# Kernel optimization log

Measured on AMD Instinct MI355X. Metric: run time of the kernel, lower is better.

Reference implementation:

```python
import math
import jax, jax.numpy as jnp
import numpy as np

H = 8
C_HIDDEN = 32
C_Q = 256


def setup_inputs() -> dict:
    key = jax.random.key(0)
    ks = jax.random.split(key, 9)
    B, S, Q, K = 1, 128, 256, 256
    q_x = jax.random.normal(ks[0], (B, S, Q, C_Q), dtype=jnp.float32)
    kv_x = jax.random.normal(ks[1], (B, S, K, C_Q), dtype=jnp.float32)
    bias1 = jax.random.normal(ks[2], (B, S, 1, 1, K), dtype=jnp.float32)
    bias2 = jax.random.normal(ks[3], (B, 1, H, Q, K), dtype=jnp.float32)
    scale = 1.0 / math.sqrt(C_Q)
    wq = jax.random.normal(ks[4], (H * C_HIDDEN, C_Q), dtype=jnp.float32) * scale
    wk = jax.random.normal(ks[5], (H * C_HIDDEN, C_Q), dtype=jnp.float32) * scale
    wv = jax.random.normal(ks[6], (H * C_HIDDEN, C_Q), dtype=jnp.float32) * scale
    wg = jax.random.normal(ks[7], (H * C_HIDDEN, C_Q), dtype=jnp.float32) * scale
    wo = jax.random.normal(ks[8], (C_Q, H * C_HIDDEN), dtype=jnp.float32) * scale
    return {"q_x": q_x, "kv_x": kv_x, "bias1": bias1, "bias2": bias2,
            "wq": wq, "wk": wk, "wv": wv, "wg": wg, "wo": wo}


def _split_heads(x):
    # [..., L, H*c] -> [..., H, L, c]
    y = x.reshape(x.shape[:-1] + (H, C_HIDDEN))
    return jnp.moveaxis(y, -2, -3)


def reference(q_x, kv_x, bias1, bias2, wq, wk, wv, wg, wo):
    # QKV projections (no bias), per-head split, scale q by 1/sqrt(c_hidden)
    q = _split_heads(q_x @ wq.T) / math.sqrt(C_HIDDEN)   # [B,S,H,Q,c]
    k = _split_heads(kv_x @ wk.T)                         # [B,S,H,K,c]
    v = _split_heads(kv_x @ wv.T)                         # [B,S,H,K,c]
    # attention logits with additive biases folded in
    a = jnp.einsum('...hqc,...hkc->...hqk', q, k) + bias1 + bias2
    a = jax.nn.softmax(a, axis=-1)
    o = jnp.einsum('...hqk,...hkc->...hqc', a, v)         # [B,S,H,Q,c]
    o = jnp.moveaxis(o, -3, -2)                           # [B,S,Q,H,c]
    # sigmoid gating from query data
    g = jax.nn.sigmoid(q_x @ wg.T)                        # [B,S,Q,H*c]
    g = g.reshape(g.shape[:-1] + (H, C_HIDDEN))
    o = o * g
    o = o.reshape(o.shape[:-2] + (H * C_HIDDEN,))         # flatten heads
    return o @ wo.T                                       # [B,S,Q,C_Q]
```

## Files before the change

### kernel.cpp

```cpp
#include <hip/hip_runtime.h>
#include <math.h>

#define S_DIM 128
#define H_DIM 8
#define M_TOT (S_DIM * 256)

typedef unsigned short ushort_t;
typedef unsigned int   uint32;
typedef __bf16  v8bf  __attribute__((ext_vector_type(8)));
typedef float   v4f   __attribute__((ext_vector_type(4)));

__device__ inline ushort_t f2b(float x) {
    unsigned int u = __float_as_uint(x);
    u += 0x7fffu + ((u >> 16) & 1u);
    return (ushort_t)(u >> 16);
}
__device__ inline float b2f(ushort_t h) {
    return __uint_as_float(((unsigned int)h) << 16);
}

#define GLDS16(gp, lp) __builtin_amdgcn_global_load_lds( \
    (const __attribute__((address_space(1))) void*)(gp), \
    (__attribute__((address_space(3))) void*)(lp), 16, 0, 0)

__global__ __launch_bounds__(256) void split_x(
    const float* __restrict__ xq, const float* __restrict__ xkv,
    ushort_t* __restrict__ hi, ushort_t* __restrict__ lo)
{
    const size_t BUF4 = (size_t)M_TOT * 64;
    const float* src = blockIdx.y ? xkv : xq;
    size_t base = (size_t)blockIdx.y * BUF4;
    int i = blockIdx.x * 256 + threadIdx.x;
    float4 v = ((const float4*)src)[i];
    ushort4 h, l;
    h.x = f2b(v.x); l.x = f2b(v.x - b2f(h.x));
    h.y = f2b(v.y); l.y = f2b(v.y - b2f(h.y));
    h.z = f2b(v.z); l.z = f2b(v.z - b2f(h.z));
    h.w = f2b(v.w); l.w = f2b(v.w - b2f(h.w));
    ((ushort4*)hi)[base + i] = h;
    ((ushort4*)lo)[base + i] = l;
}

__global__ __launch_bounds__(256) void split_w(
    const float* __restrict__ w0, const float* __restrict__ w1,
    const float* __restrict__ w2, const float* __restrict__ w3,
    const float* __restrict__ w4,
    ushort_t* __restrict__ hi, ushort_t* __restrict__ lo)
{
    const float* src;
    switch (blockIdx.y) {
        case 0: src = w0; break; case 1: src = w1; break;
        case 2: src = w2; break; case 3: src = w3; break;
        default: src = w4; break;
    }
    int i = blockIdx.x * 256 + threadIdx.x;
    float4 v = ((const float4*)src)[i];
    ushort4 h, l;
    h.x = f2b(v.x); l.x = f2b(v.x - b2f(h.x));
    h.y = f2b(v.y); l.y = f2b(v.y - b2f(h.y));
    h.z = f2b(v.z); l.z = f2b(v.z - b2f(h.z));
    h.w = f2b(v.w); l.w = f2b(v.w - b2f(h.w));
    size_t base = (size_t)blockIdx.y * 16384;
    ((ushort4*)hi)[base + i] = h;
    ((ushort4*)lo)[base + i] = l;
}


__global__ __launch_bounds__(256) void gemm_proj(
    const ushort_t* __restrict__ Xhi, const ushort_t* __restrict__ Xlo,
    const ushort_t* __restrict__ Whi4, const ushort_t* __restrict__ Wlo4,
    ushort_t* __restrict__ qh, ushort_t* __restrict__ ql,
    ushort_t* __restrict__ kh, ushort_t* __restrict__ kl,
    float* __restrict__ g_out,
    ushort_t* __restrict__ vh,
    float qscale)
{
    __shared__ ushort_t lds[4][128 * 32];

    const int z    = blockIdx.z;
    const int L    = blockIdx.x + 4 * blockIdx.y;
    const int mti  = ((L >> 5) << 3) + (L & 7);
    const int nti  = (L >> 3) & 3;
    const int t    = threadIdx.x;
    const int l    = t & 63;
    const int wv   = t >> 6;
    const int wm   = wv & 1;
    const int wn   = wv >> 1;
    const int idx  = l & 15;
    const int quad = l >> 4;
    const int m0   = mti * 128;
    const int n0   = nti * 128;

    const size_t BUF = (size_t)M_TOT * 256;
    const ushort_t* Ahi = Xhi + (size_t)z * BUF;
    const ushort_t* Alo = Xlo + (size_t)z * BUF;
    const ushort_t* Whi = Whi4 + (size_t)z * 131072;
    const ushort_t* Wlo = Wlo4 + (size_t)z * 131072;
    const float scale = z ? 1.f : qscale;

    const ushort_t* srcs[4] = { Ahi + (size_t)m0 * 256, Alo + (size_t)m0 * 256,
                                Whi + (size_t)n0 * 256, Wlo + (size_t)n0 * 256 };

    v4f acc[4][4];
    #pragma unroll
    for (int i = 0; i < 4; ++i)
        #pragma unroll
        for (int j = 0; j < 4; ++j) acc[i][j] = (v4f){0.f, 0.f, 0.f, 0.f};

    for (int k0 = 0; k0 < 256; k0 += 32) {
        #pragma unroll
        for (int b = 0; b < 4; ++b) {
            #pragma unroll
            for (int i = 0; i < 2; ++i) {
                const int sb   = wv * 128 + i * 64;
                const int slot = sb + l;
                const int row  = slot >> 2;
                const int gseg = ((slot & 3) - (row >> 1)) & 3;
                const ushort_t* g = srcs[b] + (size_t)row * 256 + k0 + gseg * 8;
                GLDS16(g, &lds[b][sb * 8]);
            }
        }
        __builtin_amdgcn_s_waitcnt(0);
        __syncthreads();

        v8bf ah[4], al[4], bh[4], bl[4];
        #pragma unroll
        for (int mt = 0; mt < 4; ++mt) {
            const int r   = wm * 64 + mt * 16 + idx;
            const int off = r * 32 + (((quad + (r >> 1)) & 3) << 3);
            ah[mt] = *(const v8bf*)&lds[0][off];
            al[mt] = *(const v8bf*)&lds[1][off];
        }
        #pragma unroll
        for (int nt = 0; nt < 4; ++nt) {
            const int r   = wn * 64 + nt * 16 + idx;
            const int off = r * 32 + (((quad + (r >> 1)) & 3) << 3);
            bh[nt] = *(const v8bf*)&lds[2][off];
            bl[nt] = *(const v8bf*)&lds[3][off];
        }

        #pragma unroll
        for (int mt = 0; mt < 4; ++mt)
            #pragma unroll
            for (int nt = 0; nt < 4; ++nt) {
                acc[mt][nt] = __builtin_amdgcn_mfma_f32_16x16x32_bf16(ah[mt], bh[nt], acc[mt][nt], 0, 0, 0);
                acc[mt][nt] = __builtin_amdgcn_mfma_f32_16x16x32_bf16(al[mt], bh[nt], acc[mt][nt], 0, 0, 0);
                acc[mt][nt] = __builtin_amdgcn_mfma_f32_16x16x32_bf16(ah[mt], bl[nt], acc[mt][nt], 0, 0, 0);
            }
        __syncthreads();
    }

    ushort_t* dsth = z ? kh : qh;
    ushort_t* dstl = z ? kl : ql;

    #pragma unroll
    for (int mt = 0; mt < 4; ++mt) {
        const int mbase = m0 + wm * 64 + mt * 16 + quad * 4;
        const int s = mbase >> 8, r8 = mbase & 255;
        #pragma unroll
        for (int nt = 0; nt < 4; ++nt) {
            const int gcol = n0 + wn * 64 + nt * 16 + idx;
            if (gcol < 256) {
                const int hh = gcol >> 5, c = gcol & 31;
                const size_t di = (((size_t)(s * 8 + hh) * 256) + r8) * 32 + c;
                #pragma unroll
                for (int r = 0; r < 4; ++r) {
                    const float val = acc[mt][nt][r] * scale;
                    const ushort_t hv = f2b(val);
                    dsth[di + (size_t)r * 32] = hv;
                    dstl[di + (size_t)r * 32] = f2b(val - b2f(hv));
                }
            } else if (z == 0) {
                const int gc = gcol - 256;
                #pragma unroll
                for (int r = 0; r < 4; ++r)
                    g_out[(size_t)(mbase + r) * 256 + gc] = acc[mt][nt][r];
            } else {
                const int gc = gcol - 256, hh = gc >> 5, c = gc & 31;
                ushort4 hv4;
                #pragma unroll
                for (int r = 0; r < 4; ++r)
                    ((ushort_t*)&hv4)[r] = f2b(acc[mt][nt][r]);
                const size_t di = (((size_t)(s * 8 + hh) * 32) + c) * 256 + r8;
                *(ushort4*)&vh[di] = hv4;
            }
        }
    }
}

__global__ __launch_bounds__(256) void gemm_out(
    const ushort_t* __restrict__ Ah, const ushort_t* __restrict__ Whi,
    const ushort_t* __restrict__ Wlo, float* __restrict__ Cf)
{
    __shared__ ushort_t lds[3][128 * 32];

    const int L    = blockIdx.x + 2 * blockIdx.y;
    const int mti  = ((L >> 4) << 3) + (L & 7);
    const int nti  = (L >> 3) & 1;
    const int t    = threadIdx.x;
    const int l    = t & 63;
    const int wv   = t >> 6;
    const int wm   = wv & 1;
    const int wn   = wv >> 1;
    const int idx  = l & 15;
    const int quad = l >> 4;
    const int m0   = mti * 128;
    const int n0   = nti * 128;

    const ushort_t* srcs[3] = { Ah + (size_t)m0 * 256,
                                Whi + (size_t)n0 * 256, Wlo + (size_t)n0 * 256 };

    v4f acc[4][4];
    #pragma unroll
    for (int i = 0; i < 4; ++i)
        #pragma unroll
        for (int j = 0; j < 4; ++j) acc[i][j] = (v4f){0.f, 0.f, 0.f, 0.f};

    for (int k0 = 0; k0 < 256; k0 += 32) {
        #pragma unroll
        for (int b = 0; b < 3; ++b) {
            #pragma unroll
            for (int i = 0; i < 2; ++i) {
                const int sb   = wv * 128 + i * 64;
                const int slot = sb + l;
                const int row  = slot >> 2;
                const int gseg = ((slot & 3) - (row >> 1)) & 3;
                const ushort_t* g = srcs[b] + (size_t)row * 256 + k0 + gseg * 8;
                GLDS16(g, &lds[b][sb * 8]);
            }
        }
        __builtin_amdgcn_s_waitcnt(0);
        __syncthreads();

        v8bf ah[4], bh[4], bl[4];
        #pragma unroll
        for (int mt = 0; mt < 4; ++mt) {
            const int r   = wm * 64 + mt * 16 + idx;
            const int off = r * 32 + (((quad + (r >> 1)) & 3) << 3);
            ah[mt] = *(const v8bf*)&lds[0][off];
        }
        #pragma unroll
        for (int nt = 0; nt < 4; ++nt) {
            const int r   = wn * 64 + nt * 16 + idx;
            const int off = r * 32 + (((quad + (r >> 1)) & 3) << 3);
            bh[nt] = *(const v8bf*)&lds[1][off];
            bl[nt] = *(const v8bf*)&lds[2][off];
        }

        #pragma unroll
        for (int mt = 0; mt < 4; ++mt)
            #pragma unroll
            for (int nt = 0; nt < 4; ++nt) {
                acc[mt][nt] = __builtin_amdgcn_mfma_f32_16x16x32_bf16(ah[mt], bh[nt], acc[mt][nt], 0, 0, 0);
                acc[mt][nt] = __builtin_amdgcn_mfma_f32_16x16x32_bf16(ah[mt], bl[nt], acc[mt][nt], 0, 0, 0);
            }
        __syncthreads();
    }

    #pragma unroll
    for (int mt = 0; mt < 4; ++mt) {
        #pragma unroll
        for (int nt = 0; nt < 4; ++nt) {
            const int gcol = n0 + wn * 64 + nt * 16 + idx;
            #pragma unroll
            for (int r = 0; r < 4; ++r) {
                const int grow = m0 + wm * 64 + mt * 16 + quad * 4 + r;
                Cf[(size_t)grow * 256 + gcol] = acc[mt][nt][r];
            }
        }
    }
}

__global__ __launch_bounds__(256, 2) void attn_mfma(
    const ushort_t* __restrict__ qh, const ushort_t* __restrict__ ql,
    const ushort_t* __restrict__ kh, const ushort_t* __restrict__ kl,
    const ushort_t* __restrict__ vth,
    const float* __restrict__ b1, const float* __restrict__ b2,
    const float* __restrict__ gbuf,
    ushort_t* __restrict__ oh)
{
    __shared__ __align__(16) uint32   pbuf[4][64 * 36];
    __shared__ __align__(16) ushort_t kst[2][3][2048];
    __shared__ __align__(16) float    invl[4][64];

    const int sh = blockIdx.x, s = sh >> 3, h = sh & 7;
    const int t = threadIdx.x, l = t & 63, w = t >> 6;
    const int idx = l & 15, quad = l >> 4;

    const size_t shb = (size_t)sh * 8192;
    const ushort_t* qhp = qh + shb;
    const ushort_t* qlp = ql + shb;
    const ushort_t* khp = kh + shb;
    const ushort_t* klp = kl + shb;
    const ushort_t* vhp = vth + shb;
    const float* b1p = b1 + (size_t)s * 256;
    const float* b2p = b2 + (size_t)h * 65536;

    const int ksrow = t >> 2;
    const int ksseg = (( (t & 3) - (ksrow >> 1)) & 3);
    const int vsrow = t >> 3;
    const int vsseg = (( (t & 7) - (vsrow >> 1)) & 7);
    const size_t koff = (size_t)ksrow * 32 + ksseg * 8;
    const size_t voff = (size_t)vsrow * 256 + vsseg * 8;
    const int wbase = w * 512;

    v8bf qfh[4], qfl[4];
    #pragma unroll
    for (int nt = 0; nt < 4; ++nt) {
        const int off = (w * 64 + nt * 16 + idx) * 32 + quad * 8;
        qfh[nt] = *(const v8bf*)(qhp + off);
        qfl[nt] = *(const v8bf*)(qlp + off);
    }

    v4f oacc[4][2];
    #pragma unroll
    for (int mt = 0; mt < 4; ++mt) {
        oacc[mt][0] = (v4f){0.f, 0.f, 0.f, 0.f};
        oacc[mt][1] = (v4f){0.f, 0.f, 0.f, 0.f};
    }
    float lrun[4] = {0.f, 0.f, 0.f, 0.f};

    GLDS16(khp + koff, &kst[0][0][wbase]);
    GLDS16(klp + koff, &kst[0][1][wbase]);
    GLDS16(vhp + voff, &kst[0][2][wbase]);
    __builtin_amdgcn_s_waitcnt(0);
    __syncthreads();

    for (int c4 = 0; c4 < 4; ++c4) {
        const int ak0 = c4 * 64;
        const int cur = c4 & 1;

        if (c4 < 3) {
            const size_t nb = (size_t)(ak0 + 64) * 32;
            GLDS16(khp + nb + koff, &kst[cur ^ 1][0][wbase]);
            GLDS16(klp + nb + koff, &kst[cur ^ 1][1][wbase]);
            GLDS16(vhp + (ak0 + 64) + voff, &kst[cur ^ 1][2][wbase]);
        }

        v8bf kfh[4], kfl[4];
        #pragma unroll
        for (int at = 0; at < 4; ++at) {
            const int row = at * 16 + idx;
            const int off = row * 32 + (((quad + (row >> 1)) & 3) << 3);
            kfh[at] = *(const v8bf*)&kst[cur][0][off];
            kfl[at] = *(const v8bf*)&kst[cur][1][off];
        }

        v4f sacc[4][4];
        #pragma unroll
        for (int at = 0; at < 4; ++at)
            #pragma unroll
            for (int nt = 0; nt < 4; ++nt)
                sacc[at][nt] = (v4f){0.f, 0.f, 0.f, 0.f};
        __builtin_amdgcn_s_setprio(1);
        #pragma unroll
        for (int at = 0; at < 4; ++at)
            #pragma unroll
            for (int nt = 0; nt < 4; ++nt) {
                sacc[at][nt] = __builtin_amdgcn_mfma_f32_16x16x32_bf16(kfh[at], qfh[nt], sacc[at][nt], 0, 0, 0);
                sacc[at][nt] = __builtin_amdgcn_mfma_f32_16x16x32_bf16(kfl[at], qfh[nt], sacc[at][nt], 0, 0, 0);
                sacc[at][nt] = __builtin_amdgcn_mfma_f32_16x16x32_bf16(kfh[at], qfl[nt], sacc[at][nt], 0, 0, 0);
            }
        __builtin_amdgcn_s_setprio(0);

        v8bf vfh[2][2];
        #pragma unroll
        for (int n2 = 0; n2 < 2; ++n2)
            #pragma unroll
            for (int kt = 0; kt < 2; ++kt) {
                const int c  = n2 * 16 + idx;
                const int sp = ((kt * 4 + quad) + (c >> 1)) & 7;
                vfh[n2][kt] = *(const v8bf*)&kst[cur][2][c * 64 + sp * 8];
            }

        v4f b1v[4];
        #pragma unroll
        for (int at = 0; at < 4; ++at)
            b1v[at] = *(const v4f*)(b1p + ak0 + at * 16 + quad * 4);

        #pragma unroll
        for (int at = 0; at < 4; ++at)
            #pragma unroll
            for (int nt = 0; nt < 4; ++nt) {
                const int q = w * 64 + nt * 16 + idx;
                v4f b2v = *(const v4f*)(b2p + (size_t)q * 256 + ak0 + at * 16 + quad * 4);
                float e0 = __expf(b1v[at][0] + b2v[0] + sacc[at][nt][0]);
                float e1 = __expf(b1v[at][1] + b2v[1] + sacc[at][nt][1]);
                float e2 = __expf(b1v[at][2] + b2v[2] + sacc[at][nt][2]);
                float e3 = __expf(b1v[at][3] + b2v[3] + sacc[at][nt][3]);
                lrun[nt] += (e0 + e1) + (e2 + e3);
                uint32 p0 = __builtin_amdgcn_perm(__float_as_uint(e1) + 0x8000u,
                                                  __float_as_uint(e0) + 0x8000u, 0x07060302u);
                uint32 p1 = __builtin_amdgcn_perm(__float_as_uint(e3) + 0x8000u,
                                                  __float_as_uint(e2) + 0x8000u, 0x07060302u);
                const int dw = (nt * 16 + idx) * 36 + at * 8 + quad * 2;
                *(uint2*)&pbuf[w][dw] = make_uint2(p0, p1);
            }

        __builtin_amdgcn_s_setprio(1);
        #pragma unroll
        for (int mt = 0; mt < 4; ++mt)
            #pragma unroll
            for (int kt = 0; kt < 2; ++kt) {
                v8bf pf = *(const v8bf*)&pbuf[w][(mt * 16 + idx) * 36 + kt * 16 + quad * 4];
                #pragma unroll
                for (int n2 = 0; n2 < 2; ++n2)
                    oacc[mt][n2] = __builtin_amdgcn_mfma_f32_16x16x32_bf16(pf, vfh[n2][kt], oacc[mt][n2], 0, 0, 0);
            }
        __builtin_amdgcn_s_setprio(0);

        __builtin_amdgcn_s_waitcnt(0);
        __syncthreads();
    }

    #pragma unroll
    for (int nt = 0; nt < 4; ++nt) {
        float v = lrun[nt];
        v += __shfl_xor(v, 16, 64);
        v += __shfl_xor(v, 32, 64);
        if (quad == 0) invl[w][nt * 16 + idx] = 1.f / v;
    }

    #pragma unroll
    for (int mt = 0; mt < 4; ++mt) {
        v4f iv = *(const v4f*)&invl[w][mt * 16 + quad * 4];
        #pragma unroll
        for (int n2 = 0; n2 < 2; ++n2) {
            const int c = n2 * 16 + idx;
            #pragma unroll
            for (int r = 0; r < 4; ++r) {
                const int q = w * 64 + mt * 16 + quad * 4 + r;
                const size_t gi = (size_t)(s * 256 + q) * 256 + h * 32 + c;
                const float gv = gbuf[gi];
                const float sig = 1.f / (1.f + __expf(-gv));
                oh[gi] = f2b(oacc[mt][n2][r] * iv[r] * sig);
            }
        }
    }
}

extern "C" void kernel_launch(void* const* d_in, const int* in_sizes, int n_in,
                              void* d_out, int out_size, void* d_ws, size_t ws_size,
                              hipStream_t stream)
{
    const float* q_x   = (const float*)d_in[0];
    const float* kv_x  = (const float*)d_in[1];
    const float* bias1 = (const float*)d_in[2];
    const float* bias2 = (const float*)d_in[3];
    const float* wq    = (const float*)d_in[4];
    const float* wk    = (const float*)d_in[5];
    const float* wv    = (const float*)d_in[6];
    const float* wg    = (const float*)d_in[7];
    const float* wo    = (const float*)d_in[8];
    float* out = (float*)d_out;

    const size_t BUF = (size_t)M_TOT * 256;

    float*    g_buf = (float*)d_ws;
    ushort_t* p     = (ushort_t*)(g_buf + BUF);
    ushort_t* qhb = p;            ushort_t* qlb = qhb + BUF;
    ushort_t* khb = qlb + BUF;    ushort_t* klb = khb + BUF;
    ushort_t* vhb = klb + BUF;
    ushort_t* ohb = vhb + BUF;
    ushort_t* xhb = ohb + BUF;    ushort_t* xlb = xhb + 2 * BUF;
    ushort_t* w_hi = xlb + 2 * BUF;
    ushort_t* w_lo = w_hi + 5 * 65536;

    const float qscale = 0.17677669529663689f;

    split_w<<<dim3(64, 5), 256, 0, stream>>>(wq, wg, wk, wv, wo, w_hi, w_lo);

    split_x<<<dim3(8192, 2), 256, 0, stream>>>(q_x, kv_x, xhb, xlb);

    gemm_proj<<<dim3(4, 256, 2), 256, 0, stream>>>(
        xhb, xlb, w_hi, w_lo, qhb, qlb, khb, klb, g_buf, vhb, qscale);

    attn_mfma<<<S_DIM * H_DIM, 256, 0, stream>>>(
        qhb, qlb, khb, klb, vhb, bias1, bias2, g_buf, ohb);

    gemm_out<<<dim3(2, 256), 256, 0, stream>>>(
        ohb, w_hi + 4 * 65536, w_lo + 4 * 65536, out);
}
```

Before: 269.2 us.

## Double-buffer LDS tiles in projection GEMMs and re-layout V staging in attention

```diff
diff --git a/kernel.cpp b/kernel.cpp
--- a/kernel.cpp
+++ b/kernel.cpp
@@ -75,7 +75,7 @@
     ushort_t* __restrict__ vh,
     float qscale)
 {
-    __shared__ ushort_t lds[4][128 * 32];
+    __shared__ ushort_t lds[2][4][128 * 32];
 
     const int z    = blockIdx.z;
     const int L    = blockIdx.x + 4 * blockIdx.y;
@@ -101,42 +101,58 @@
     const ushort_t* srcs[4] = { Ahi + (size_t)m0 * 256, Alo + (size_t)m0 * 256,
                                 Whi + (size_t)n0 * 256, Wlo + (size_t)n0 * 256 };
 
+    size_t stoff[2]; int sdst[2];
+    #pragma unroll
+    for (int i = 0; i < 2; ++i) {
+        const int sb   = wv * 128 + i * 64;
+        const int slot = sb + l;
+        const int row  = slot >> 2;
+        const int gseg = ((slot & 3) - (row >> 1)) & 3;
+        stoff[i] = (size_t)row * 256 + gseg * 8;
+        sdst[i]  = sb * 8;
+    }
+
     v4f acc[4][4];
     #pragma unroll
     for (int i = 0; i < 4; ++i)
         #pragma unroll
         for (int j = 0; j < 4; ++j) acc[i][j] = (v4f){0.f, 0.f, 0.f, 0.f};
 
+    const int ra  = wm * 64 + 0 * 16 + idx;
+    (void)ra;
+
+    #pragma unroll
+    for (int b = 0; b < 4; ++b)
+        #pragma unroll
+        for (int i = 0; i < 2; ++i)
+            GLDS16(srcs[b] + stoff[i], &lds[0][b][sdst[i]]);
+    __builtin_amdgcn_s_waitcnt(0);
+    __syncthreads();
+
+    int cur = 0;
     for (int k0 = 0; k0 < 256; k0 += 32) {
-        #pragma unroll
-        for (int b = 0; b < 4; ++b) {
-            #pragma unroll
-            for (int i = 0; i < 2; ++i) {
-                const int sb   = wv * 128 + i * 64;
-                const int slot = sb + l;
-                const int row  = slot >> 2;
-                const int gseg = ((slot & 3) - (row >> 1)) & 3;
-                const ushort_t* g = srcs[b] + (size_t)row * 256 + k0 + gseg * 8;
-                GLDS16(g, &lds[b][sb * 8]);
-            }
-        }
-        __builtin_amdgcn_s_waitcnt(0);
-        __syncthreads();
+        if (k0 < 224) {
+            #pragma unroll
+            for (int b = 0; b < 4; ++b)
+                #pragma unroll
+                for (int i = 0; i < 2; ++i)
+                    GLDS16(srcs[b] + stoff[i] + k0 + 32, &lds[cur ^ 1][b][sdst[i]]);
+        }
 
         v8bf ah[4], al[4], bh[4], bl[4];
         #pragma unroll
         for (int mt = 0; mt < 4; ++mt) {
             const int r   = wm * 64 + mt * 16 + idx;
             const int off = r * 32 + (((quad + (r >> 1)) & 3) << 3);
-            ah[mt] = *(const v8bf*)&lds[0][off];
-            al[mt] = *(const v8bf*)&lds[1][off];
+            ah[mt] = *(const v8bf*)&lds[cur][0][off];
+            al[mt] = *(const v8bf*)&lds[cur][1][off];
         }
         #pragma unroll
         for (int nt = 0; nt < 4; ++nt) {
             const int r   = wn * 64 + nt * 16 + idx;
             const int off = r * 32 + (((quad + (r >> 1)) & 3) << 3);
-            bh[nt] = *(const v8bf*)&lds[2][off];
-            bl[nt] = *(const v8bf*)&lds[3][off];
+            bh[nt] = *(const v8bf*)&lds[cur][2][off];
+            bl[nt] = *(const v8bf*)&lds[cur][3][off];
         }
 
         #pragma unroll
@@ -147,7 +163,10 @@
                 acc[mt][nt] = __builtin_amdgcn_mfma_f32_16x16x32_bf16(al[mt], bh[nt], acc[mt][nt], 0, 0, 0);
                 acc[mt][nt] = __builtin_amdgcn_mfma_f32_16x16x32_bf16(ah[mt], bl[nt], acc[mt][nt], 0, 0, 0);
             }
+
+        __builtin_amdgcn_s_waitcnt(0);
         __syncthreads();
+        cur ^= 1;
     }
 
     ushort_t* dsth = z ? kh : qh;
@@ -192,7 +211,7 @@
     const ushort_t* __restrict__ Ah, const ushort_t* __restrict__ Whi,
     const ushort_t* __restrict__ Wlo, float* __restrict__ Cf)
 {
-    __shared__ ushort_t lds[3][128 * 32];
+    __shared__ ushort_t lds[2][3][128 * 32];
 
     const int L    = blockIdx.x + 2 * blockIdx.y;
     const int mti  = ((L >> 4) << 3) + (L & 7);
@@ -210,41 +229,54 @@
     const ushort_t* srcs[3] = { Ah + (size_t)m0 * 256,
                                 Whi + (size_t)n0 * 256, Wlo + (size_t)n0 * 256 };
 
+    size_t stoff[2]; int sdst[2];
+    #pragma unroll
+    for (int i = 0; i < 2; ++i) {
+        const int sb   = wv * 128 + i * 64;
+        const int slot = sb + l;
+        const int row  = slot >> 2;
+        const int gseg = ((slot & 3) - (row >> 1)) & 3;
+        stoff[i] = (size_t)row * 256 + gseg * 8;
+        sdst[i]  = sb * 8;
+    }
+
     v4f acc[4][4];
     #pragma unroll
     for (int i = 0; i < 4; ++i)
         #pragma unroll
         for (int j = 0; j < 4; ++j) acc[i][j] = (v4f){0.f, 0.f, 0.f, 0.f};
 
+    #pragma unroll
+    for (int b = 0; b < 3; ++b)
+        #pragma unroll
+        for (int i = 0; i < 2; ++i)
+            GLDS16(srcs[b] + stoff[i], &lds[0][b][sdst[i]]);
+    __builtin_amdgcn_s_waitcnt(0);
+    __syncthreads();
+
+    int cur = 0;
     for (int k0 = 0; k0 < 256; k0 += 32) {
-        #pragma unroll
-        for (int b = 0; b < 3; ++b) {
-            #pragma unroll
-            for (int i = 0; i < 2; ++i) {
-                const int sb   = wv * 128 + i * 64;
-                const int slot = sb + l;
-                const int row  = slot >> 2;
-                const int gseg = ((slot & 3) - (row >> 1)) & 3;
-                const ushort_t* g = srcs[b] + (size_t)row * 256 + k0 + gseg * 8;
-                GLDS16(g, &lds[b][sb * 8]);
-            }
-        }
-        __builtin_amdgcn_s_waitcnt(0);
-        __syncthreads();
+        if (k0 < 224) {
+            #pragma unroll
+            for (int b = 0; b < 3; ++b)
+                #pragma unroll
+                for (int i = 0; i < 2; ++i)
+                    GLDS16(srcs[b] + stoff[i] + k0 + 32, &lds[cur ^ 1][b][sdst[i]]);
+        }
 
         v8bf ah[4], bh[4], bl[4];
         #pragma unroll
         for (int mt = 0; mt < 4; ++mt) {
             const int r   = wm * 64 + mt * 16 + idx;
             const int off = r * 32 + (((quad + (r >> 1)) & 3) << 3);
-            ah[mt] = *(const v8bf*)&lds[0][off];
+            ah[mt] = *(const v8bf*)&lds[cur][0][off];
         }
         #pragma unroll
         for (int nt = 0; nt < 4; ++nt) {
             const int r   = wn * 64 + nt * 16 + idx;
             const int off = r * 32 + (((quad + (r >> 1)) & 3) << 3);
-            bh[nt] = *(const v8bf*)&lds[1][off];
-            bl[nt] = *(const v8bf*)&lds[2][off];
+            bh[nt] = *(const v8bf*)&lds[cur][1][off];
+            bl[nt] = *(const v8bf*)&lds[cur][2][off];
         }
 
         #pragma unroll
@@ -254,7 +286,10 @@
                 acc[mt][nt] = __builtin_amdgcn_mfma_f32_16x16x32_bf16(ah[mt], bh[nt], acc[mt][nt], 0, 0, 0);
                 acc[mt][nt] = __builtin_amdgcn_mfma_f32_16x16x32_bf16(ah[mt], bl[nt], acc[mt][nt], 0, 0, 0);
             }
+
+        __builtin_amdgcn_s_waitcnt(0);
         __syncthreads();
+        cur ^= 1;
     }
 
     #pragma unroll
@@ -297,11 +332,12 @@
     const float* b2p = b2 + (size_t)h * 65536;
 
     const int ksrow = t >> 2;
-    const int ksseg = (( (t & 3) - (ksrow >> 1)) & 3);
-    const int vsrow = t >> 3;
-    const int vsseg = (( (t & 7) - (vsrow >> 1)) & 7);
+    const int ksseg = ((t & 3) - (ksrow >> 1)) & 3;
     const size_t koff = (size_t)ksrow * 32 + ksseg * 8;
-    const size_t voff = (size_t)vsrow * 256 + vsseg * 8;
+    const int vc   = (t >> 2) & 31;
+    const int vkt  = t >> 7;
+    const int vseg = ((t & 3) - (vc >> 1)) & 3;
+    const size_t voff = (size_t)vc * 256 + vkt * 32 + vseg * 8;
     const int wbase = w * 512;
 
     v8bf qfh[4], qfl[4];
@@ -369,8 +405,8 @@
             #pragma unroll
             for (int kt = 0; kt < 2; ++kt) {
                 const int c  = n2 * 16 + idx;
-                const int sp = ((kt * 4 + quad) + (c >> 1)) & 7;
-                vfh[n2][kt] = *(const v8bf*)&kst[cur][2][c * 64 + sp * 8];
+                const int sp = (quad + (c >> 1)) & 3;
+                vfh[n2][kt] = *(const v8bf*)&kst[cur][2][kt * 1024 + c * 32 + sp * 8];
             }
 
         v4f b1v[4];
```

Result: no change. 264.0 us (-1.9%).
